# Optimization experiments

Hardware: AMD Instinct MI355X
Metric: run time of the kernel (lower is better)

The kernel has to match this reference:

```python
import jax, jax.numpy as jnp
import numpy as np

N, D_IN, D_OUT, E, TOPK = 2048, 2048, 2048, 8, 2


def setup_inputs() -> dict:
    key = jax.random.key(0)
    k1, k2, k3, k4 = jax.random.split(key, 4)
    inputs = jax.random.normal(k1, (N, D_IN), dtype=jnp.float32)
    weight = jax.random.normal(k2, (E, D_OUT, D_IN), dtype=jnp.float32) * (1.0 / np.sqrt(D_IN))
    gates = jax.random.uniform(k3, (N, TOPK), dtype=jnp.float32)
    gates = gates / jnp.sum(gates, axis=-1, keepdims=True)
    # random routing: expert id for each of the N*TOPK (token, slot) pairs
    expert_of = jax.random.randint(k4, (N * TOPK,), 0, E, dtype=jnp.int32)
    order = jnp.argsort(expert_of)  # positions sorted by expert id
    sorted_expert_idxs = expert_of[order].astype(jnp.int32)
    sorted_scattered_idxs = order.astype(jnp.int32)
    counts = jnp.bincount(expert_of, length=E)
    expert_offsets = jnp.cumsum(counts).astype(jnp.int32)
    padded_block_idxs = jnp.zeros((1,), dtype=jnp.int32)  # kernel blocking artifact, no math effect
    return {
        "inputs": inputs,
        "weight": weight,
        "k": TOPK,
        "sorted_expert_idxs": sorted_expert_idxs,
        "sorted_scattered_idxs": sorted_scattered_idxs,
        "padded_block_idxs": padded_block_idxs,
        "expert_offsets": expert_offsets,
        "gates": gates,
    }


def reference(inputs, weight, k, sorted_expert_idxs, sorted_scattered_idxs,
              padded_block_idxs, expert_offsets, gates):
    # inputs: [N, d_in]; weight: [E, d_out, d_in] (module permutes to [E, d_in, d_out])
    n_tok, d_in = inputs.shape
    n_e, d_out, _ = weight.shape
    nk = sorted_expert_idxs.shape[0]
    # invert the sort: expert id per flat (token, slot) position
    expert_of = jnp.zeros((nk,), dtype=sorted_expert_idxs.dtype).at[sorted_scattered_idxs].set(sorted_expert_idxs)
    x_flat = inputs[jnp.arange(nk) // k]  # [N*k, d_in] (fan-out of k per token)
    # grouped GEMM: y_flat[j] = x_flat[j] @ weight[expert_of[j]].T
    y_flat = jnp.zeros((nk, d_out), dtype=inputs.dtype)
    for e in range(n_e):  # loop over fixed small expert count (structural)
        mask = (expert_of == e)[:, None]
        y_flat = y_flat + jnp.where(mask, x_flat, 0.0) @ weight[e].T
    # gating combine: bmm(gates[:, None, :], y.view(N, k, d_out))
    out = jnp.einsum('nk,nkd->nd', gates, y_flat.reshape(n_tok, k, d_out))
    return out
```

## Files before the change

kernel.cpp:

```cpp
#include <hip/hip_runtime.h>
#include <hip/hip_bf16.h>

#define DIN   2048
#define DOUT  2048
#define NTOK  2048
#define NE    8
#define TOPK  2
#define NK    (NTOK*TOPK)
#define BM    128
#define BN    128
#define BK    64
#define KTILES (DIN/BK)
#define MAXMT  (NK/BM + NE)

typedef __attribute__((ext_vector_type(8))) short bf16x8;
typedef __attribute__((ext_vector_type(4))) float f32x4;

__device__ inline unsigned pack2rn(float a, float b) {
    union { float f; unsigned u; } x, y; x.f = a; y.f = b;
    return __builtin_amdgcn_perm(y.u + 0x8000u, x.u + 0x8000u, 0x07060302u);
}

__global__ __launch_bounds__(256, 3) void moe_gemm(
    const float* __restrict__ inputs,
    const float* __restrict__ weight,
    const int*   __restrict__ sorted_scattered_idxs,
    const int*   __restrict__ expert_offsets,
    const float* __restrict__ gates,
    float*       __restrict__ out)
{
    __shared__ unsigned short As[BM * BK];
    __shared__ unsigned short Bs[BN * BK];
    __shared__ int   s_tok[BM];
    __shared__ float s_gate[BM];

    const int mt = blockIdx.y;
    const int n0 = blockIdx.x * BN;

    int e = -1, m0 = 0, cnt = 0;
    {
        int acc = 0, prev = 0;
        for (int i = 0; i < NE; ++i) {
            int end = expert_offsets[i];
            int c = end - prev;
            int t = (c + BM - 1) / BM;
            if (mt < acc + t) {
                e = i; m0 = prev + (mt - acc) * BM;
                cnt = end - m0; if (cnt > BM) cnt = BM;
                break;
            }
            acc += t; prev = end;
        }
    }
    if (e < 0) return;

    const int tid = threadIdx.x;
    if (tid < BM) {
        int idx = (tid < cnt) ? (m0 + tid) : m0;
        int p = sorted_scattered_idxs[idx];
        s_tok[tid]  = p;
        s_gate[tid] = gates[p];
    }
    __syncthreads();

    const int ch  = tid & 7;
    const int r0  = tid >> 3;
    const int sch = ch ^ (r0 & 7);

    const float* wbase = weight + (size_t)e * DOUT * DIN;
    const float* ap[4];
    const float* bp[4];
    #pragma unroll
    for (int i = 0; i < 4; ++i) {
        int r = r0 + 32 * i;
        ap[i] = inputs + (size_t)(s_tok[r] >> 1) * DIN + ch * 8;
        bp[i] = wbase + (size_t)(n0 + r) * DIN + ch * 8;
    }
    unsigned short* aw = &As[r0 * BK + sch * 8];
    unsigned short* bw = &Bs[r0 * BK + sch * 8];

    const int wid = tid >> 6, lane = tid & 63;
    const int wm = (wid >> 1) * 64, wn = (wid & 1) * 64;
    const int g  = lane >> 4, lr = lane & 15;

    f32x4 acc[4][4];
    #pragma unroll
    for (int i = 0; i < 4; ++i)
        #pragma unroll
        for (int j = 0; j < 4; ++j) acc[i][j] = (f32x4)0.0f;

    float4 pa[4][2], pb[4][2];
    #pragma unroll
    for (int i = 0; i < 4; ++i) {
        pa[i][0] = *(const float4*)(ap[i] + 0);
        pa[i][1] = *(const float4*)(ap[i] + 4);
        pb[i][0] = *(const float4*)(bp[i] + 0);
        pb[i][1] = *(const float4*)(bp[i] + 4);
    }

    for (int kt = 0; kt < KTILES; ++kt) {
        __syncthreads();
        #pragma unroll
        for (int i = 0; i < 4; ++i) {
            uint4 va, vb;
            va.x = pack2rn(pa[i][0].x, pa[i][0].y);
            va.y = pack2rn(pa[i][0].z, pa[i][0].w);
            va.z = pack2rn(pa[i][1].x, pa[i][1].y);
            va.w = pack2rn(pa[i][1].z, pa[i][1].w);
            *(uint4*)(aw + i * 32 * BK) = va;
            vb.x = pack2rn(pb[i][0].x, pb[i][0].y);
            vb.y = pack2rn(pb[i][0].z, pb[i][0].w);
            vb.z = pack2rn(pb[i][1].x, pb[i][1].y);
            vb.w = pack2rn(pb[i][1].z, pb[i][1].w);
            *(uint4*)(bw + i * 32 * BK) = vb;
        }
        __syncthreads();
        if (kt + 1 < KTILES) {
            const int kof = (kt + 1) * BK;
            #pragma unroll
            for (int i = 0; i < 4; ++i) {
                pa[i][0] = *(const float4*)(ap[i] + kof);
                pa[i][1] = *(const float4*)(ap[i] + kof + 4);
                pb[i][0] = *(const float4*)(bp[i] + kof);
                pb[i][1] = *(const float4*)(bp[i] + kof + 4);
            }
        }
        #pragma unroll
        for (int ks = 0; ks < 2; ++ks) {
            bf16x8 a[4], b[4];
            #pragma unroll
            for (int i = 0; i < 4; ++i) {
                int ra = wm + i * 16 + lr;
                int ca = (ks * 4 + g) ^ (ra & 7);
                a[i] = *(const bf16x8*)(&As[ra * BK + ca * 8]);
                int rb = wn + i * 16 + lr;
                int cb = (ks * 4 + g) ^ (rb & 7);
                b[i] = *(const bf16x8*)(&Bs[rb * BK + cb * 8]);
            }
            #pragma unroll
            for (int i = 0; i < 4; ++i)
                #pragma unroll
                for (int j = 0; j < 4; ++j)
                    acc[i][j] = __builtin_amdgcn_mfma_f32_16x16x32_bf16(a[i], b[j], acc[i][j], 0, 0, 0);
        }
    }

    #pragma unroll
    for (int i = 0; i < 4; ++i) {
        #pragma unroll
        for (int j2 = 0; j2 < 4; ++j2) {
            int lrow = wm + i * 16 + g * 4 + j2;
            if (lrow < cnt) {
                int   p  = s_tok[lrow];
                float gf = s_gate[lrow];
                float* orow = out + (size_t)(p >> 1) * DOUT + n0 + wn;
                #pragma unroll
                for (int nf = 0; nf < 4; ++nf)
                    atomicAdd(orow + nf * 16 + lr, gf * acc[i][nf][j2]);
            }
        }
    }
}

extern "C" void kernel_launch(void* const* d_in, const int* in_sizes, int n_in,
                              void* d_out, int out_size, void* d_ws, size_t ws_size,
                              hipStream_t stream) {
    const float* inputs  = (const float*)d_in[0];
    const float* weight  = (const float*)d_in[1];
    const int*   ssi     = (const int*)d_in[4];
    const int*   eoff    = (const int*)d_in[6];
    const float* gates   = (const float*)d_in[7];
    float* out = (float*)d_out;

    hipMemsetAsync(out, 0, (size_t)out_size * sizeof(float), stream);
    dim3 grid(DOUT / BN, MAXMT);
    moe_gemm<<<grid, 256, 0, stream>>>(inputs, weight, ssi, eoff, gates, out);
}
```

Before: 111.0 us.

## Pre-convert weights and inputs to bf16, then GEMM with async global-to-LDS double buffering

Adds a separate kernel that converts the whole fp32 weight tensor and the inputs to bf16 in workspace. The GEMM kernel then streams bf16 tiles directly into LDS with global_load_lds and a double buffer, removing the per-tile register pack and convert and one barrier per k-step. In exchange it adds a full extra read of the fp32 weights plus a bf16 write and re-read each call. The old fused kernel is kept as a fallback when the workspace is too small.

```diff
diff --git a/kernel.cpp b/kernel.cpp
--- a/kernel.cpp
+++ b/kernel.cpp
@@ -13,24 +13,53 @@
 #define KTILES (DIN/BK)
 #define MAXMT  (NK/BM + NE)
 
+#define WEL   (NE*DOUT*DIN)
+#define XEL   (NTOK*DIN)
+
+typedef unsigned short u16;
 typedef __attribute__((ext_vector_type(8))) short bf16x8;
 typedef __attribute__((ext_vector_type(4))) float f32x4;
 
-__device__ inline unsigned pack2rn(float a, float b) {
+__device__ __forceinline__ unsigned pack2rn(float a, float b) {
     union { float f; unsigned u; } x, y; x.f = a; y.f = b;
     return __builtin_amdgcn_perm(y.u + 0x8000u, x.u + 0x8000u, 0x07060302u);
 }
 
-__global__ __launch_bounds__(256, 3) void moe_gemm(
-    const float* __restrict__ inputs,
-    const float* __restrict__ weight,
-    const int*   __restrict__ sorted_scattered_idxs,
-    const int*   __restrict__ expert_offsets,
+__device__ __forceinline__ void gl_lds16(const void* g, void* l) {
+    __builtin_amdgcn_global_load_lds(
+        (const __attribute__((address_space(1))) void*)g,
+        (__attribute__((address_space(3)))       void*)l, 16, 0, 0);
+}
+
+__global__ __launch_bounds__(256) void cvt_bf16(
+    const float* __restrict__ w, const float* __restrict__ x,
+    u16* __restrict__ wbf, u16* __restrict__ xbf)
+{
+    const size_t nch = (size_t)(WEL + XEL) / 8;
+    for (size_t c = (size_t)blockIdx.x * blockDim.x + threadIdx.x; c < nch;
+         c += (size_t)gridDim.x * blockDim.x) {
+        const float* src; u16* dst; size_t off;
+        if (c < (size_t)WEL / 8) { src = w; dst = wbf; off = c * 8; }
+        else                     { src = x; dst = xbf; off = (c - (size_t)WEL / 8) * 8; }
+        float4 f0 = *(const float4*)(src + off);
+        float4 f1 = *(const float4*)(src + off + 4);
+        uint4 pk;
+        pk.x = pack2rn(f0.x, f0.y); pk.y = pack2rn(f0.z, f0.w);
+        pk.z = pack2rn(f1.x, f1.y); pk.w = pack2rn(f1.z, f1.w);
+        *(uint4*)(dst + off) = pk;
+    }
+}
+
+__global__ __launch_bounds__(256, 2) void moe_gemm_split(
+    const u16* __restrict__ xb,
+    const u16* __restrict__ wb,
+    const int* __restrict__ sorted_scattered_idxs,
+    const int* __restrict__ expert_offsets,
     const float* __restrict__ gates,
-    float*       __restrict__ out)
+    float*     __restrict__ out)
 {
-    __shared__ unsigned short As[BM * BK];
-    __shared__ unsigned short Bs[BN * BK];
+    __shared__ u16 As[2][BM * BK];
+    __shared__ u16 Bs[2][BN * BK];
     __shared__ int   s_tok[BM];
     __shared__ float s_gate[BM];
 
@@ -63,25 +92,31 @@
     }
     __syncthreads();
 
-    const int ch  = tid & 7;
-    const int r0  = tid >> 3;
-    const int sch = ch ^ (r0 & 7);
-
-    const float* wbase = weight + (size_t)e * DOUT * DIN;
-    const float* ap[4];
-    const float* bp[4];
-    #pragma unroll
-    for (int i = 0; i < 4; ++i) {
-        int r = r0 + 32 * i;
-        ap[i] = inputs + (size_t)(s_tok[r] >> 1) * DIN + ch * 8;
-        bp[i] = wbase + (size_t)(n0 + r) * DIN + ch * 8;
-    }
-    unsigned short* aw = &As[r0 * BK + sch * 8];
-    unsigned short* bw = &Bs[r0 * BK + sch * 8];
-
     const int wid = tid >> 6, lane = tid & 63;
+
+    const u16* wbase = wb + (size_t)e * DOUT * DIN;
+    const u16* aSrc[4];
+    const u16* bSrc[4];
+    #pragma unroll
+    for (int s = 0; s < 4; ++s) {
+        int r  = wid * 32 + s * 8 + (lane >> 3);
+        int cg = (lane & 7) ^ (r & 7);
+        aSrc[s] = xb + (size_t)(s_tok[r] >> 1) * DIN + cg * 8;
+        bSrc[s] = wbase + (size_t)(n0 + r) * DIN + cg * 8;
+    }
+    const int segoff = wid * 32 * BK;
+
+    const int g = lane >> 4, lr = lane & 15;
     const int wm = (wid >> 1) * 64, wn = (wid & 1) * 64;
-    const int g  = lane >> 4, lr = lane & 15;
+    int aoff[2][4], boff[2][4];
+    #pragma unroll
+    for (int ks = 0; ks < 2; ++ks)
+        #pragma unroll
+        for (int i = 0; i < 4; ++i) {
+            int cc = (ks * 4 + g) ^ (lr & 7);
+            aoff[ks][i] = (wm + i * 16 + lr) * BK + cc * 8;
+            boff[ks][i] = (wn + i * 16 + lr) * BK + cc * 8;
+        }
 
     f32x4 acc[4][4];
     #pragma unroll
@@ -89,40 +124,21 @@
         #pragma unroll
         for (int j = 0; j < 4; ++j) acc[i][j] = (f32x4)0.0f;
 
-    float4 pa[4][2], pb[4][2];
-    #pragma unroll
-    for (int i = 0; i < 4; ++i) {
-        pa[i][0] = *(const float4*)(ap[i] + 0);
-        pa[i][1] = *(const float4*)(ap[i] + 4);
-        pb[i][0] = *(const float4*)(bp[i] + 0);
-        pb[i][1] = *(const float4*)(bp[i] + 4);
-    }
-
+    #pragma unroll
+    for (int s = 0; s < 4; ++s) {
+        gl_lds16(aSrc[s], &As[0][segoff + s * 8 * BK]);
+        gl_lds16(bSrc[s], &Bs[0][segoff + s * 8 * BK]);
+    }
+    __syncthreads();
+
+    int cur = 0;
     for (int kt = 0; kt < KTILES; ++kt) {
-        __syncthreads();
-        #pragma unroll
-        for (int i = 0; i < 4; ++i) {
-            uint4 va, vb;
-            va.x = pack2rn(pa[i][0].x, pa[i][0].y);
-            va.y = pack2rn(pa[i][0].z, pa[i][0].w);
-            va.z = pack2rn(pa[i][1].x, pa[i][1].y);
-            va.w = pack2rn(pa[i][1].z, pa[i][1].w);
-            *(uint4*)(aw + i * 32 * BK) = va;
-            vb.x = pack2rn(pb[i][0].x, pb[i][0].y);
-            vb.y = pack2rn(pb[i][0].z, pb[i][0].w);
-            vb.z = pack2rn(pb[i][1].x, pb[i][1].y);
-            vb.w = pack2rn(pb[i][1].z, pb[i][1].w);
-            *(uint4*)(bw + i * 32 * BK) = vb;
-        }
-        __syncthreads();
         if (kt + 1 < KTILES) {
             const int kof = (kt + 1) * BK;
             #pragma unroll
-            for (int i = 0; i < 4; ++i) {
-                pa[i][0] = *(const float4*)(ap[i] + kof);
-                pa[i][1] = *(const float4*)(ap[i] + kof + 4);
-                pb[i][0] = *(const float4*)(bp[i] + kof);
-                pb[i][1] = *(const float4*)(bp[i] + kof + 4);
+            for (int s = 0; s < 4; ++s) {
+                gl_lds16(aSrc[s] + kof, &As[cur ^ 1][segoff + s * 8 * BK]);
+                gl_lds16(bSrc[s] + kof, &Bs[cur ^ 1][segoff + s * 8 * BK]);
             }
         }
         #pragma unroll
@@ -130,12 +146,8 @@
             bf16x8 a[4], b[4];
             #pragma unroll
             for (int i = 0; i < 4; ++i) {
-                int ra = wm + i * 16 + lr;
-                int ca = (ks * 4 + g) ^ (ra & 7);
-                a[i] = *(const bf16x8*)(&As[ra * BK + ca * 8]);
-                int rb = wn + i * 16 + lr;
-                int cb = (ks * 4 + g) ^ (rb & 7);
-                b[i] = *(const bf16x8*)(&Bs[rb * BK + cb * 8]);
+                a[i] = *(const bf16x8*)(&As[cur][aoff[ks][i]]);
+                b[i] = *(const bf16x8*)(&Bs[cur][boff[ks][i]]);
             }
             #pragma unroll
             for (int i = 0; i < 4; ++i)
@@ -143,6 +155,8 @@
                 for (int j = 0; j < 4; ++j)
                     acc[i][j] = __builtin_amdgcn_mfma_f32_16x16x32_bf16(a[i], b[j], acc[i][j], 0, 0, 0);
         }
+        __syncthreads();
+        cur ^= 1;
     }
 
     #pragma unroll
@@ -162,6 +176,129 @@
     }
 }
 
+__global__ __launch_bounds__(256, 3) void moe_gemm_fused(
+    const float* __restrict__ inputs, const float* __restrict__ weight,
+    const int* __restrict__ sorted_scattered_idxs, const int* __restrict__ expert_offsets,
+    const float* __restrict__ gates, float* __restrict__ out)
+{
+    __shared__ u16 As[BM * BK];
+    __shared__ u16 Bs[BN * BK];
+    __shared__ int   s_tok[BM];
+    __shared__ float s_gate[BM];
+
+    const int mt = blockIdx.y;
+    const int n0 = blockIdx.x * BN;
+    int e = -1, m0 = 0, cnt = 0;
+    {
+        int acc = 0, prev = 0;
+        for (int i = 0; i < NE; ++i) {
+            int end = expert_offsets[i];
+            int c = end - prev;
+            int t = (c + BM - 1) / BM;
+            if (mt < acc + t) {
+                e = i; m0 = prev + (mt - acc) * BM;
+                cnt = end - m0; if (cnt > BM) cnt = BM;
+                break;
+            }
+            acc += t; prev = end;
+        }
+    }
+    if (e < 0) return;
+
+    const int tid = threadIdx.x;
+    if (tid < BM) {
+        int idx = (tid < cnt) ? (m0 + tid) : m0;
+        int p = sorted_scattered_idxs[idx];
+        s_tok[tid]  = p;
+        s_gate[tid] = gates[p];
+    }
+    __syncthreads();
+
+    const int ch  = tid & 7;
+    const int r0  = tid >> 3;
+    const int sch = ch ^ (r0 & 7);
+    const float* wbase = weight + (size_t)e * DOUT * DIN;
+    const float* ap[4]; const float* bp[4];
+    #pragma unroll
+    for (int i = 0; i < 4; ++i) {
+        int r = r0 + 32 * i;
+        ap[i] = inputs + (size_t)(s_tok[r] >> 1) * DIN + ch * 8;
+        bp[i] = wbase + (size_t)(n0 + r) * DIN + ch * 8;
+    }
+    u16* aw = &As[r0 * BK + sch * 8];
+    u16* bw = &Bs[r0 * BK + sch * 8];
+
+    const int wid = tid >> 6, lane = tid & 63;
+    const int wm = (wid >> 1) * 64, wn = (wid & 1) * 64;
+    const int g  = lane >> 4, lr = lane & 15;
+
+    f32x4 acc[4][4];
+    #pragma unroll
+    for (int i = 0; i < 4; ++i)
+        #pragma unroll
+        for (int j = 0; j < 4; ++j) acc[i][j] = (f32x4)0.0f;
+
+    float4 pa[4][2], pb[4][2];
+    #pragma unroll
+    for (int i = 0; i < 4; ++i) {
+        pa[i][0] = *(const float4*)(ap[i] + 0); pa[i][1] = *(const float4*)(ap[i] + 4);
+        pb[i][0] = *(const float4*)(bp[i] + 0); pb[i][1] = *(const float4*)(bp[i] + 4);
+    }
+    for (int kt = 0; kt < KTILES; ++kt) {
+        __syncthreads();
+        #pragma unroll
+        for (int i = 0; i < 4; ++i) {
+            uint4 va, vb;
+            va.x = pack2rn(pa[i][0].x, pa[i][0].y); va.y = pack2rn(pa[i][0].z, pa[i][0].w);
+            va.z = pack2rn(pa[i][1].x, pa[i][1].y); va.w = pack2rn(pa[i][1].z, pa[i][1].w);
+            *(uint4*)(aw + i * 32 * BK) = va;
+            vb.x = pack2rn(pb[i][0].x, pb[i][0].y); vb.y = pack2rn(pb[i][0].z, pb[i][0].w);
+            vb.z = pack2rn(pb[i][1].x, pb[i][1].y); vb.w = pack2rn(pb[i][1].z, pb[i][1].w);
+            *(uint4*)(bw + i * 32 * BK) = vb;
+        }
+        __syncthreads();
+        if (kt + 1 < KTILES) {
+            const int kof = (kt + 1) * BK;
+            #pragma unroll
+            for (int i = 0; i < 4; ++i) {
+                pa[i][0] = *(const float4*)(ap[i] + kof); pa[i][1] = *(const float4*)(ap[i] + kof + 4);
+                pb[i][0] = *(const float4*)(bp[i] + kof); pb[i][1] = *(const float4*)(bp[i] + kof + 4);
+            }
+        }
+        #pragma unroll
+        for (int ks = 0; ks < 2; ++ks) {
+            bf16x8 a[4], b[4];
+            #pragma unroll
+            for (int i = 0; i < 4; ++i) {
+                int ra = wm + i * 16 + lr; int ca = (ks * 4 + g) ^ (ra & 7);
+                a[i] = *(const bf16x8*)(&As[ra * BK + ca * 8]);
+                int rb = wn + i * 16 + lr; int cb = (ks * 4 + g) ^ (rb & 7);
+                b[i] = *(const bf16x8*)(&Bs[rb * BK + cb * 8]);
+            }
+            #pragma unroll
+            for (int i = 0; i < 4; ++i)
+                #pragma unroll
+                for (int j = 0; j < 4; ++j)
+                    acc[i][j] = __builtin_amdgcn_mfma_f32_16x16x32_bf16(a[i], b[j], acc[i][j], 0, 0, 0);
+        }
+    }
+    #pragma unroll
+    for (int i = 0; i < 4; ++i) {
+        #pragma unroll
+        for (int j2 = 0; j2 < 4; ++j2) {
+            int lrow = wm + i * 16 + g * 4 + j2;
+            if (lrow < cnt) {
+                int   p  = s_tok[lrow];
+                float gf = s_gate[lrow];
+                float* orow = out + (size_t)(p >> 1) * DOUT + n0 + wn;
+                #pragma unroll
+                for (int nf = 0; nf < 4; ++nf)
+                    atomicAdd(orow + nf * 16 + lr, gf * acc[i][nf][j2]);
+            }
+        }
+    }
+}
+
 extern "C" void kernel_launch(void* const* d_in, const int* in_sizes, int n_in,
                               void* d_out, int out_size, void* d_ws, size_t ws_size,
                               hipStream_t stream) {
@@ -174,5 +311,14 @@
 
     hipMemsetAsync(out, 0, (size_t)out_size * sizeof(float), stream);
     dim3 grid(DOUT / BN, MAXMT);
-    moe_gemm<<<grid, 256, 0, stream>>>(inputs, weight, ssi, eoff, gates, out);
-}
+
+    const size_t need = ((size_t)WEL + (size_t)XEL) * sizeof(u16);
+    if (ws_size >= need) {
+        u16* wbf = (u16*)d_ws;
+        u16* xbf = wbf + (size_t)WEL;
+        cvt_bf16<<<2048, 256, 0, stream>>>(weight, inputs, wbf, xbf);
+        moe_gemm_split<<<grid, 256, 0, stream>>>(xbf, wbf, ssi, eoff, gates, out);
+    } else {
+        moe_gemm_fused<<<grid, 256, 0, stream>>>(inputs, weight, ssi, eoff, gates, out);
+    }
+}
```

Result: slower. 131.3 us (+18.3%).
